# Kernel tuning notes

Measured on AMD Instinct MI355X. Metric: run time of the kernel, lower is better.

## Reference

```python
import jax, jax.numpy as jnp
import numpy as np

N, E, C1, E2, C2, B = 30000, 400000, 15000, 100000, 7500, 16
FV, FE, NC = 6, 3, 10


def _lin(k, i, o):
    kw, kb = jax.random.split(k)
    s = 1.0 / np.sqrt(i)
    w = jax.random.uniform(kw, (i, o), jnp.float32, -s, s)
    b = jax.random.uniform(kb, (o,), jnp.float32, -s, s)
    return w, b


def setup_inputs() -> dict:
    key = jax.random.key(0)
    ks = jax.random.split(key, 20)
    inp = {}
    inp["x"] = jax.random.normal(ks[0], (N, FV), jnp.float32)
    inp["edge_attr"] = jax.random.uniform(ks[1], (E, FE), jnp.float32)
    inp["pos"] = jax.random.uniform(ks[2], (N, 3), jnp.float32)
    inp["edge_index"] = jax.random.randint(ks[3], (2, E), 0, N)
    inp["batch"] = jnp.sort(jax.random.randint(ks[4], (N,), 0, B))
    inp["cluster1"] = jax.random.randint(ks[5], (N,), 0, C1)
    inp["edge_index2"] = jax.random.randint(ks[6], (2, E2), 0, C1)
    inp["cluster2"] = jax.random.randint(ks[7], (C1,), 0, C2)
    inp["w1a"], inp["b1a"] = _lin(ks[8], FE, 25)
    inp["w1b"], inp["b1b"] = _lin(ks[9], 25, 32 * FV)
    inp["root1"] = jax.random.normal(ks[10], (FV, 32), jnp.float32) / np.sqrt(FV)
    inp["bias1"] = jnp.zeros((32,), jnp.float32)
    inp["w2a"], inp["b2a"] = _lin(ks[11], 3, 25)
    inp["w2b"], inp["b2b"] = _lin(ks[12], 25, 32 * 64)
    inp["root2"] = jax.random.normal(ks[13], (32, 64), jnp.float32) / np.sqrt(32)
    inp["bias2"] = jnp.zeros((64,), jnp.float32)
    inp["fc1_w"], inp["fc1_b"] = _lin(ks[14], 64, 128)
    inp["fc2_w"], inp["fc2_b"] = _lin(ks[15], 128, NC)
    return inp


def _seg_mean(v, idx, n):
    s = jax.ops.segment_sum(v, idx, num_segments=n)
    c = jax.ops.segment_sum(jnp.ones(idx.shape, v.dtype), idx, num_segments=n)
    return s / jnp.maximum(c, 1.0)[:, None]


def _seg_max(v, idx, n):
    m = jax.ops.segment_max(v, idx, num_segments=n)
    return jnp.where(jnp.isfinite(m), m, 0.0)  # empty clusters -> 0


def _nnconv(x, src, dst, ea, wa, ba, wb, bb, root, bias, n, ci, co):
    # per-edge weight matrix from edge MLP: [E, ci, co]
    W = (jax.nn.relu(ea @ wa + ba) @ wb + bb).reshape(-1, ci, co)
    msg = jnp.einsum('ei,eio->eo', x[src], W)  # gather + per-edge matmul
    return _seg_mean(msg, dst, n) + x @ root + bias  # scatter-mean + root


def _cartesian(pos, src, dst):
    cart = pos[src] - pos[dst]
    return cart / (2.0 * jnp.max(jnp.abs(cart))) + 0.5  # T.Cartesian(norm=True)


def reference(x, edge_attr, pos, w1a, b1a, w1b, b1b, root1, bias1,
              w2a, b2a, w2b, b2b, root2, bias2, fc1_w, fc1_b, fc2_w, fc2_b,
              edge_index, batch, cluster1, edge_index2, cluster2):
    src1, dst1 = edge_index[0], edge_index[1]
    x1 = jax.nn.elu(_nnconv(x, src1, dst1, edge_attr, w1a, b1a, w1b, b1b,
                            root1, bias1, N, FV, 32))
    # max_pool with precomputed graclus cluster assignment
    xp = _seg_max(x1, cluster1, C1)
    posp = _seg_mean(pos, cluster1, C1)
    batchp = jnp.maximum(jax.ops.segment_max(batch, cluster1, num_segments=C1), 0)
    src2, dst2 = edge_index2[0], edge_index2[1]
    ea2 = _cartesian(posp, src2, dst2)
    x2 = jax.nn.elu(_nnconv(xp, src2, dst2, ea2, w2a, b2a, w2b, b2b,
                            root2, bias2, C1, 32, 64))
    # max_pool_x with second cluster assignment
    x3 = _seg_max(x2, cluster2, C2)
    batch2 = jnp.maximum(jax.ops.segment_max(batchp, cluster2, num_segments=C2), 0)
    g = _seg_mean(x3, batch2, B)  # global mean pool -> [B, 64]
    h = jax.nn.elu(g @ fc1_w + fc1_b)
    # dropout is identity in eval mode
    return jax.nn.log_softmax(h @ fc2_w + fc2_b, axis=1)
```

## Files before the change

kernel.cpp:

```cpp
#include <hip/hip_runtime.h>
#include <hip/hip_bf16.h>

#define Nn 30000
#define Ee 400000
#define C1n 15000
#define E2n 100000
#define C2n 7500
#define Bb 16

#define OFF_XPKEY   0
#define OFF_POSSUM  480000
#define OFF_CNTC1   525000
#define OFF_BPMAX   540000
#define OFF_X3KEY   555000
#define OFF_B2MAX   1035000
#define OFF_GSUM    1042500
#define OFF_GCNT    1043524
#define OFF_MAXABS  1043540
#define OFF_DEG1    1043544
#define OFF_FILL1   1073544
#define OFF_DEG2    1103544
#define OFF_FILL2   1118544
#define ZERO_ELEMS  1133544
#define OFF_RP1     1133544
#define OFF_RP2     1163548
#define OFF_POSP    1178552
#define OFF_XP      1223552
#define OFF_W1T     1703552
#define OFF_W2T     1707136
#define OFF_EA1R    1735808
#define OFF_C2R     3335808

typedef __attribute__((ext_vector_type(8))) short short8;
typedef __attribute__((ext_vector_type(4))) float f32x4;

__device__ __forceinline__ unsigned fkey(float f) {
    unsigned u = __float_as_uint(f);
    return (u >> 31) ? ~u : (u | 0x80000000u);
}
__device__ __forceinline__ float funkey(unsigned k) {
    unsigned u = (k >> 31) ? (k ^ 0x80000000u) : ~k;
    return __uint_as_float(u);
}
__device__ __forceinline__ float elu(float a) { return a > 0.f ? a : expm1f(a); }

__device__ __forceinline__ unsigned short f2bf(float f) {
    unsigned u = __float_as_uint(f);
    unsigned lsb = (u >> 16) & 1u;
    u += 0x7fffu + lsb;
    return (unsigned short)(u >> 16);
}

__global__ void hist_kernel(const int* __restrict__ ei, const int* __restrict__ ei2,
                            unsigned* __restrict__ deg1, unsigned* __restrict__ deg2) {
    int t = blockIdx.x * 256 + threadIdx.x;
    if (t < Ee) {
        atomicAdd(&deg1[ei[Ee + t]], 1u);
    } else if (t < Ee + E2n) {
        int e = t - Ee;
        atomicAdd(&deg2[ei2[E2n + e]], 1u);
    }
}

__global__ __launch_bounds__(1024) void scan_both(
    const unsigned* __restrict__ deg1, unsigned* __restrict__ rp1,
    const unsigned* __restrict__ deg2, unsigned* __restrict__ rp2) {
    const unsigned* deg; unsigned* rp; int n;
    if (blockIdx.x == 0) { deg = deg1; rp = rp1; n = Nn; }
    else                 { deg = deg2; rp = rp2; n = C1n; }
    __shared__ unsigned ps[1024];
    const int t = threadIdx.x;
    const int chunk = (n + 1023) / 1024;
    const int lo = t * chunk;
    const int hi = (lo + chunk < n) ? lo + chunk : n;
    unsigned s = 0;
    for (int i = lo; i < hi; ++i) s += deg[i];
    ps[t] = s;
    __syncthreads();
    for (int off = 1; off < 1024; off <<= 1) {
        unsigned v = (t >= off) ? ps[t - off] : 0u;
        __syncthreads();
        ps[t] += v;
        __syncthreads();
    }
    unsigned run = (t > 0) ? ps[t - 1] : 0u;
    if (t == 0) rp[0] = 0u;
    for (int i = lo; i < hi; ++i) { run += deg[i]; rp[i + 1] = run; }
}

__global__ void scatter1(const float* __restrict__ ea, const int* __restrict__ ei,
                         const unsigned* __restrict__ rp1, unsigned* __restrict__ fill1,
                         float4* __restrict__ EA1R) {
    int e = blockIdx.x * 256 + threadIdx.x;
    if (e >= Ee) return;
    int d = ei[Ee + e];
    unsigned p = rp1[d] + atomicAdd(&fill1[d], 1u);
    int src = ei[e];
    EA1R[p] = make_float4(ea[e * 3], ea[e * 3 + 1], ea[e * 3 + 2], __int_as_float(src));
}

__global__ void wt_kernel(const float* __restrict__ w1b, const float* __restrict__ b1b,
                          const float* __restrict__ root1, const float* __restrict__ bias1,
                          const float* __restrict__ w2b, const float* __restrict__ b2b,
                          const float* __restrict__ root2, const float* __restrict__ bias2,
                          unsigned short* __restrict__ W1T, unsigned short* __restrict__ W2T) {
    int t = blockIdx.x * 256 + threadIdx.x;
    if (t < 32 * 224) {
        int col = t / 224, p = t % 224;
        float v = 0.f;
        if (p < 208) {
            int k = p >> 3, i = p & 7;
            if (i < 6) v = (k < 25) ? w1b[k * 192 + i * 32 + col] : b1b[i * 32 + col];
        }
        else if (p < 214)  { v = root1[(p - 208) * 32 + col]; }
        else if (p == 214) { v = bias1[col]; }
        W1T[t] = f2bf(v);
    } else {
        int u = t - 32 * 224;
        if (u < 64 * 896) {
            int col = u / 896, p = u % 896;
            float v;
            if (p < 800)       { int k = p / 32, i = p % 32; v = w2b[k * 2048 + i * 64 + col]; }
            else if (p < 832)  { int i = p - 800; v = b2b[i * 64 + col]; }
            else if (p < 864)  { v = root2[(p - 832) * 64 + col]; }
            else if (p == 864) { v = bias2[col]; }
            else v = 0.f;
            W2T[u] = f2bf(v);
        }
    }
}

__global__ __launch_bounds__(256, 8) void g1conv1(
    const float* __restrict__ x, const float4* __restrict__ EA1R,
    const unsigned* __restrict__ rp1,
    const float* __restrict__ w1a, const float* __restrict__ b1a,
    const unsigned short* __restrict__ W1T,
    const float* __restrict__ pos, const int* __restrict__ batch, const int* __restrict__ cl1,
    unsigned* __restrict__ xpkey, float* __restrict__ possum,
    float* __restrict__ cntc1, int* __restrict__ bpmax) {
    __shared__ unsigned short As[16][232];
    const int tid = threadIdx.x;
    const int w = tid >> 6;
    const int l = tid & 63;
    const int m = l & 15, q = l >> 4;
    const int i8 = l & 7;
    const int kq = l >> 3;
    float wa0 = 0.f, wa1 = 0.f, wa2 = 0.f, ba0 = 0.f;
    if (l < 25) { wa0 = w1a[l]; wa1 = w1a[25 + l]; wa2 = w1a[50 + l]; ba0 = b1a[l]; }
    const int ntiles = Nn / 16;
    for (int tile = blockIdx.x; tile < ntiles; tile += gridDim.x) {
        const int base = tile * 16;
#pragma unroll
        for (int s4 = 0; s4 < 4; ++s4) {
            const int row = w * 4 + s4;
            const int d = base + row;
            const unsigned e0 = rp1[d], e1 = rp1[d + 1];
            float acc0 = 0.f, acc1 = 0.f, acc2 = 0.f, acc3 = 0.f;
            for (unsigned p = e0; p < e1; p += 4) {
                float4 ev[4];
                float xm[4];
#pragma unroll
                for (int b = 0; b < 4; ++b) {
                    const unsigned pp = (p + b < e1) ? p + b : e1 - 1;
                    ev[b] = EA1R[pp];
                }
#pragma unroll
                for (int b = 0; b < 4; ++b) {
                    const int sb = __float_as_int(ev[b].w) * 6;
                    xm[b] = (i8 < 6 && p + b < e1) ? x[sb + i8] : 0.f;
                }
#pragma unroll
                for (int b = 0; b < 4; ++b) {
                    float a = ba0 + ev[b].x * wa0 + ev[b].y * wa1 + ev[b].z * wa2;
                    float hown = (l == 25) ? 1.f : fmaxf(a, 0.f);
                    acc0 += __shfl(hown, kq, 64) * xm[b];
                    acc1 += __shfl(hown, 8 + kq, 64) * xm[b];
                    acc2 += __shfl(hown, 16 + kq, 64) * xm[b];
                    acc3 += __shfl(hown, 24 + kq, 64) * xm[b];
                }
            }
            const float dinv = 1.f / fmaxf((float)(e1 - e0), 1.f);
            As[row][l] = f2bf(acc0 * dinv);
            As[row][64 + l] = f2bf(acc1 * dinv);
            As[row][128 + l] = f2bf(acc2 * dinv);
            if (l < 16) {
                As[row][192 + l] = f2bf(acc3 * dinv);
                float tail;
                if (l < 6)       tail = x[d * 6 + l];
                else if (l == 6) tail = 1.f;
                else             tail = 0.f;
                As[row][208 + l] = f2bf(tail);
            }
        }
        __syncthreads();
        if (w < 2) {
            f32x4 acc = {0.f, 0.f, 0.f, 0.f};
#pragma unroll
            for (int s = 0; s < 7; ++s) {
                short8 av = *reinterpret_cast<const short8*>(&As[m][s * 32 + q * 8]);
                short8 bv = *reinterpret_cast<const short8*>(&W1T[(w * 16 + m) * 224 + s * 32 + q * 8]);
                acc = __builtin_amdgcn_mfma_f32_16x16x32_bf16(av, bv, acc, 0, 0, 0);
            }
#pragma unroll
            for (int r = 0; r < 4; ++r) {
                const int row = base + q * 4 + r;
                const int c = cl1[row];
                float v = elu(acc[r]);
                atomicMax(&xpkey[c * 32 + w * 16 + m], fkey(v));
            }
        } else if (w == 2) {
            if (l < 16) {
                const int row = base + l;
                const int c = cl1[row];
#pragma unroll
                for (int j = 0; j < 3; ++j) atomicAdd(&possum[c * 3 + j], pos[row * 3 + j]);
                atomicAdd(&cntc1[c], 1.f);
                atomicMax(&bpmax[c], batch[row]);
            }
        }
        __syncthreads();
    }
}

__global__ void pool1_final(const unsigned* __restrict__ xpkey, const float* __restrict__ possum,
                            const float* __restrict__ cntc1, float* __restrict__ xp,
                            float* __restrict__ posp) {
    int t = blockIdx.x * 256 + threadIdx.x;
    if (t >= C1n * 32) return;
    int c = t >> 5, o = t & 31;
    unsigned k = xpkey[t];
    xp[t] = k ? funkey(k) : 0.f;
    if (o < 3) posp[c * 3 + o] = possum[c * 3 + o] / fmaxf(cntc1[c], 1.f);
}

__global__ void scatter2(const float* __restrict__ posp, const int* __restrict__ ei2,
                         const unsigned* __restrict__ rp2, unsigned* __restrict__ fill2,
                         float4* __restrict__ C2R, unsigned* __restrict__ maxabs) {
    int e = blockIdx.x * 256 + threadIdx.x;
    float mx = 0.f;
    if (e < E2n) {
        int s = ei2[e], d = ei2[E2n + e];
        float c0 = posp[s * 3]     - posp[d * 3];
        float c1 = posp[s * 3 + 1] - posp[d * 3 + 1];
        float c2 = posp[s * 3 + 2] - posp[d * 3 + 2];
        mx = fmaxf(fmaxf(fabsf(c0), fabsf(c1)), fabsf(c2));
        unsigned p = rp2[d] + atomicAdd(&fill2[d], 1u);
        C2R[p] = make_float4(c0, c1, c2, __int_as_float(s));
    }
#pragma unroll
    for (int off = 32; off > 0; off >>= 1) mx = fmaxf(mx, __shfl_xor(mx, off));
    if ((threadIdx.x & 63) == 0) atomicMax(maxabs, __float_as_uint(mx));
}

__global__ __launch_bounds__(256, 5) void g2conv2(
    const float* __restrict__ xp, const float4* __restrict__ C2R,
    const unsigned* __restrict__ maxabs, const unsigned* __restrict__ rp2,
    const float* __restrict__ w2a, const float* __restrict__ b2a,
    const unsigned short* __restrict__ W2T,
    const int* __restrict__ cl2, const int* __restrict__ bpmax,
    unsigned* __restrict__ x3key, int* __restrict__ b2max) {
    __shared__ unsigned short As[16][904];
    const int tid = threadIdx.x;
    const int w = tid >> 6;
    const int l = tid & 63;
    const int m = l & 15, q = l >> 4;
    const int i = l & 31, hp = l >> 5;
    float wa0 = 0.f, wa1 = 0.f, wa2 = 0.f, ba0 = 0.f;
    if (l < 25) { wa0 = w2a[l]; wa1 = w2a[25 + l]; wa2 = w2a[50 + l]; ba0 = b2a[l]; }
    const float inv = 0.5f / __uint_as_float(maxabs[0]);
    const int ntiles = (C1n + 15) / 16;
    for (int tile = blockIdx.x; tile < ntiles; tile += gridDim.x) {
        const int base = tile * 16;
#pragma unroll
        for (int s4 = 0; s4 < 4; ++s4) {
            const int row = w * 4 + s4;
            const int d = base + row;
            if (d < C1n) {
                const unsigned e0 = rp2[d], e1 = rp2[d + 1];
                float acc[13];
#pragma unroll
                for (int r = 0; r < 13; ++r) acc[r] = 0.f;
                for (unsigned p = e0; p < e1; p += 4) {
                    float4 cv[4];
                    float xv[4];
#pragma unroll
                    for (int b = 0; b < 4; ++b) {
                        const unsigned pp = (p + b < e1) ? p + b : e1 - 1;
                        cv[b] = C2R[pp];
                    }
#pragma unroll
                    for (int b = 0; b < 4; ++b)
                        xv[b] = (p + b < e1) ? xp[__float_as_int(cv[b].w) * 32 + i] : 0.f;
#pragma unroll
                    for (int b = 0; b < 4; ++b) {
                        float a = ba0 + (cv[b].x * inv + 0.5f) * wa0 + (cv[b].y * inv + 0.5f) * wa1
                                      + (cv[b].z * inv + 0.5f) * wa2;
                        float hown = (l == 25) ? 1.f : fmaxf(a, 0.f);
#pragma unroll
                        for (int r = 0; r < 13; ++r)
                            acc[r] += __shfl(hown, 2 * r + hp, 64) * xv[b];
                    }
                }
                const float dinv = 1.f / fmaxf((float)(e1 - e0), 1.f);
#pragma unroll
                for (int r = 0; r < 13; ++r) As[row][r * 64 + l] = f2bf(acc[r] * dinv);
                As[row][832 + l] = f2bf((l < 32) ? xp[d * 32 + l] : (l == 32 ? 1.f : 0.f));
                if (l == 0) atomicMax(&b2max[cl2[d]], bpmax[d]);
            } else {
#pragma unroll
                for (int r = 0; r < 13; ++r) As[row][r * 64 + l] = 0;
                As[row][832 + l] = 0;
            }
        }
        __syncthreads();
        {
            f32x4 a4 = {0.f, 0.f, 0.f, 0.f};
#pragma unroll 4
            for (int s = 0; s < 28; ++s) {
                short8 av = *reinterpret_cast<const short8*>(&As[m][s * 32 + q * 8]);
                short8 bv = *reinterpret_cast<const short8*>(&W2T[(w * 16 + m) * 896 + s * 32 + q * 8]);
                a4 = __builtin_amdgcn_mfma_f32_16x16x32_bf16(av, bv, a4, 0, 0, 0);
            }
#pragma unroll
            for (int r = 0; r < 4; ++r) {
                const int row = base + q * 4 + r;
                if (row < C1n) {
                    const int c2 = cl2[row];
                    float v = elu(a4[r]);
                    atomicMax(&x3key[c2 * 64 + w * 16 + m], fkey(v));
                }
            }
        }
        __syncthreads();
    }
}

__global__ __launch_bounds__(256) void gacc_kernel(
    const unsigned* __restrict__ x3key, const int* __restrict__ b2max,
    float* __restrict__ gsum, float* __restrict__ gcnt) {
    __shared__ float ls[Bb * 64];
    __shared__ float lc[Bb];
    const int t = threadIdx.x;
    for (int i = t; i < Bb * 64; i += 256) ls[i] = 0.f;
    if (t < Bb) lc[t] = 0.f;
    __syncthreads();
    const int o = t & 63;
    const int cs = t >> 6;
    for (int c = blockIdx.x * 4 + cs; c < C2n; c += gridDim.x * 4) {
        int b = b2max[c];
        unsigned k = x3key[c * 64 + o];
        float v = k ? funkey(k) : 0.f;
        atomicAdd(&ls[b * 64 + o], v);
        if (o == 0) atomicAdd(&lc[b], 1.f);
    }
    __syncthreads();
    for (int i = t; i < Bb * 64; i += 256) {
        float v = ls[i];
        if (v != 0.f) atomicAdd(&gsum[i], v);
    }
    if (t < Bb) {
        float v = lc[t];
        if (v != 0.f) atomicAdd(&gcnt[t], v);
    }
}

__global__ void head_kernel(const float* __restrict__ gsum, const float* __restrict__ gcnt,
                            const float* __restrict__ fc1w, const float* __restrict__ fc1b,
                            const float* __restrict__ fc2w, const float* __restrict__ fc2b,
                            float* __restrict__ out) {
    __shared__ float g[16 * 64];
    __shared__ float hb[16 * 128];
    __shared__ float lg[16 * 10];
    __shared__ float rowm[16];
    int t = threadIdx.x;
    for (int idx = t; idx < 16 * 64; idx += 256) {
        int b = idx >> 6;
        g[idx] = gsum[idx] / fmaxf(gcnt[b], 1.f);
    }
    __syncthreads();
    for (int idx = t; idx < 16 * 128; idx += 256) {
        int b = idx >> 7, j = idx & 127;
        float a = fc1b[j];
        for (int i = 0; i < 64; ++i) a += g[b * 64 + i] * fc1w[i * 128 + j];
        hb[idx] = elu(a);
    }
    __syncthreads();
    for (int idx = t; idx < 160; idx += 256) {
        int b = idx / 10, c = idx % 10;
        float a = fc2b[c];
        for (int i = 0; i < 128; ++i) a += hb[b * 128 + i] * fc2w[i * 10 + c];
        lg[idx] = a;
    }
    __syncthreads();
    if (t < 16) {
        float m = -1e30f;
        for (int c = 0; c < 10; ++c) m = fmaxf(m, lg[t * 10 + c]);
        float s = 0.f;
        for (int c = 0; c < 10; ++c) s += expf(lg[t * 10 + c] - m);
        rowm[t] = m + logf(s);
    }
    __syncthreads();
    for (int idx = t; idx < 160; idx += 256) out[idx] = lg[idx] - rowm[idx / 10];
}

extern "C" void kernel_launch(void* const* d_in, const int* in_sizes, int n_in,
                              void* d_out, int out_size, void* d_ws, size_t ws_size,
                              hipStream_t stream) {
    const float* x     = (const float*)d_in[0];
    const float* ea    = (const float*)d_in[1];
    const float* pos   = (const float*)d_in[2];
    const int*   ei    = (const int*)d_in[3];
    const int*   batch = (const int*)d_in[4];
    const int*   cl1   = (const int*)d_in[5];
    const int*   ei2   = (const int*)d_in[6];
    const int*   cl2   = (const int*)d_in[7];
    const float* w1a   = (const float*)d_in[8];
    const float* b1a   = (const float*)d_in[9];
    const float* w1b   = (const float*)d_in[10];
    const float* b1b   = (const float*)d_in[11];
    const float* root1 = (const float*)d_in[12];
    const float* bias1 = (const float*)d_in[13];
    const float* w2a   = (const float*)d_in[14];
    const float* b2a   = (const float*)d_in[15];
    const float* w2b   = (const float*)d_in[16];
    const float* b2b   = (const float*)d_in[17];
    const float* root2 = (const float*)d_in[18];
    const float* bias2 = (const float*)d_in[19];
    const float* fc1w  = (const float*)d_in[20];
    const float* fc1b  = (const float*)d_in[21];
    const float* fc2w  = (const float*)d_in[22];
    const float* fc2b  = (const float*)d_in[23];
    float* out = (float*)d_out;

    float* ws = (float*)d_ws;
    unsigned* xpkey  = (unsigned*)(ws + OFF_XPKEY);
    float*    possum = ws + OFF_POSSUM;
    float*    cntc1  = ws + OFF_CNTC1;
    int*      bpmax  = (int*)(ws + OFF_BPMAX);
    unsigned* x3key  = (unsigned*)(ws + OFF_X3KEY);
    int*      b2max  = (int*)(ws + OFF_B2MAX);
    float*    gsum   = ws + OFF_GSUM;
    float*    gcnt   = ws + OFF_GCNT;
    unsigned* maxabs = (unsigned*)(ws + OFF_MAXABS);
    unsigned* deg1   = (unsigned*)(ws + OFF_DEG1);
    unsigned* fill1  = (unsigned*)(ws + OFF_FILL1);
    unsigned* deg2   = (unsigned*)(ws + OFF_DEG2);
    unsigned* fill2  = (unsigned*)(ws + OFF_FILL2);
    unsigned* rp1    = (unsigned*)(ws + OFF_RP1);
    unsigned* rp2    = (unsigned*)(ws + OFF_RP2);
    float*    posp   = ws + OFF_POSP;
    float*    xp     = ws + OFF_XP;
    unsigned short* W1T = (unsigned short*)(ws + OFF_W1T);
    unsigned short* W2T = (unsigned short*)(ws + OFF_W2T);
    float4*   EA1R  = (float4*)(ws + OFF_EA1R);
    float4*   C2R   = (float4*)(ws + OFF_C2R);

    hipMemsetAsync(ws, 0, (size_t)ZERO_ELEMS * 4, stream);

    wt_kernel<<<252, 256, 0, stream>>>(w1b, b1b, root1, bias1, w2b, b2b, root2, bias2, W1T, W2T);
    hist_kernel<<<(Ee + E2n + 255) / 256, 256, 0, stream>>>(ei, ei2, deg1, deg2);
    scan_both<<<2, 1024, 0, stream>>>(deg1, rp1, deg2, rp2);
    scatter1<<<(Ee + 255) / 256, 256, 0, stream>>>(ea, ei, rp1, fill1, EA1R);
    g1conv1<<<1875, 256, 0, stream>>>(x, EA1R, rp1, w1a, b1a, W1T, pos, batch, cl1,
                                      xpkey, possum, cntc1, bpmax);
    pool1_final<<<(C1n * 32 + 255) / 256, 256, 0, stream>>>(xpkey, possum, cntc1, xp, posp);
    scatter2<<<(E2n + 255) / 256, 256, 0, stream>>>(posp, ei2, rp2, fill2, C2R, maxabs);
    g2conv2<<<938, 256, 0, stream>>>(xp, C2R, maxabs, rp2, w2a, b2a, W2T, cl2, bpmax,
                                     x3key, b2max);
    gacc_kernel<<<32, 256, 0, stream>>>(x3key, b2max, gsum, gcnt);
    head_kernel<<<1, 256, 0, stream>>>(gsum, gcnt, fc1w, fc1b, fc2w, fc2b, out);
}
```

Baseline: 340.3 us.

## Pre-gather source node features into CSR-ordered edge buffers during scatter

The scatter kernels now copy each edge's source-node features (x for conv1, pooled xp for conv2) into edge-sorted buffers laid out in CSR order. The conv kernels then read these features contiguously instead of doing a dependent random gather through the source index stored in the edge record. This takes the dependent load latency out of the conv inner loops. In exchange it adds large extra writes (8 floats per edge for conv1, 32 floats per edge for conv2), and the random gathers still happen, only moved into the scatter kernels.

```diff
diff --git a/kernel.cpp b/kernel.cpp
--- a/kernel.cpp
+++ b/kernel.cpp
@@ -30,6 +30,8 @@
 #define OFF_W2T     1707136
 #define OFF_EA1R    1735808
 #define OFF_C2R     3335808
+#define OFF_X1R     3735808
+#define OFF_XP2R    6935808
 
 typedef __attribute__((ext_vector_type(8))) short short8;
 typedef __attribute__((ext_vector_type(4))) float f32x4;
@@ -88,15 +90,19 @@
     for (int i = lo; i < hi; ++i) { run += deg[i]; rp[i + 1] = run; }
 }
 
-__global__ void scatter1(const float* __restrict__ ea, const int* __restrict__ ei,
+__global__ void scatter1(const float* __restrict__ x, const float* __restrict__ ea,
+                         const int* __restrict__ ei,
                          const unsigned* __restrict__ rp1, unsigned* __restrict__ fill1,
-                         float4* __restrict__ EA1R) {
+                         float4* __restrict__ EA1R, float4* __restrict__ X1R) {
     int e = blockIdx.x * 256 + threadIdx.x;
     if (e >= Ee) return;
     int d = ei[Ee + e];
     unsigned p = rp1[d] + atomicAdd(&fill1[d], 1u);
     int src = ei[e];
-    EA1R[p] = make_float4(ea[e * 3], ea[e * 3 + 1], ea[e * 3 + 2], __int_as_float(src));
+    EA1R[p] = make_float4(ea[e * 3], ea[e * 3 + 1], ea[e * 3 + 2], 0.f);
+    const float* xs = x + (size_t)src * 6;
+    X1R[p * 2]     = make_float4(xs[0], xs[1], xs[2], xs[3]);
+    X1R[p * 2 + 1] = make_float4(xs[4], xs[5], 0.f, 0.f);
 }
 
 __global__ void wt_kernel(const float* __restrict__ w1b, const float* __restrict__ b1b,
@@ -131,8 +137,8 @@
 }
 
 __global__ __launch_bounds__(256, 8) void g1conv1(
-    const float* __restrict__ x, const float4* __restrict__ EA1R,
-    const unsigned* __restrict__ rp1,
+    const float4* __restrict__ EA1R, const float* __restrict__ X1Rf,
+    const float* __restrict__ x, const unsigned* __restrict__ rp1,
     const float* __restrict__ w1a, const float* __restrict__ b1a,
     const unsigned short* __restrict__ W1T,
     const float* __restrict__ pos, const int* __restrict__ batch, const int* __restrict__ cl1,
@@ -163,11 +169,8 @@
                 for (int b = 0; b < 4; ++b) {
                     const unsigned pp = (p + b < e1) ? p + b : e1 - 1;
                     ev[b] = EA1R[pp];
-                }
-#pragma unroll
-                for (int b = 0; b < 4; ++b) {
-                    const int sb = __float_as_int(ev[b].w) * 6;
-                    xm[b] = (i8 < 6 && p + b < e1) ? x[sb + i8] : 0.f;
+                    float xv = X1Rf[(size_t)pp * 8 + i8];
+                    xm[b] = (p + b < e1) ? xv : 0.f;
                 }
 #pragma unroll
                 for (int b = 0; b < 4; ++b) {
@@ -233,9 +236,11 @@
     if (o < 3) posp[c * 3 + o] = possum[c * 3 + o] / fmaxf(cntc1[c], 1.f);
 }
 
-__global__ void scatter2(const float* __restrict__ posp, const int* __restrict__ ei2,
+__global__ void scatter2(const float* __restrict__ posp, const float* __restrict__ xp,
+                         const int* __restrict__ ei2,
                          const unsigned* __restrict__ rp2, unsigned* __restrict__ fill2,
-                         float4* __restrict__ C2R, unsigned* __restrict__ maxabs) {
+                         float4* __restrict__ C2R, float4* __restrict__ XP2R,
+                         unsigned* __restrict__ maxabs) {
     int e = blockIdx.x * 256 + threadIdx.x;
     float mx = 0.f;
     if (e < E2n) {
@@ -245,7 +250,11 @@
         float c2 = posp[s * 3 + 2] - posp[d * 3 + 2];
         mx = fmaxf(fmaxf(fabsf(c0), fabsf(c1)), fabsf(c2));
         unsigned p = rp2[d] + atomicAdd(&fill2[d], 1u);
-        C2R[p] = make_float4(c0, c1, c2, __int_as_float(s));
+        C2R[p] = make_float4(c0, c1, c2, 0.f);
+        const float4* xs = reinterpret_cast<const float4*>(xp + (size_t)s * 32);
+        float4* xd = XP2R + (size_t)p * 8;
+#pragma unroll
+        for (int j = 0; j < 8; ++j) xd[j] = xs[j];
     }
 #pragma unroll
     for (int off = 32; off > 0; off >>= 1) mx = fmaxf(mx, __shfl_xor(mx, off));
@@ -253,7 +262,8 @@
 }
 
 __global__ __launch_bounds__(256, 5) void g2conv2(
-    const float* __restrict__ xp, const float4* __restrict__ C2R,
+    const float4* __restrict__ C2R, const float* __restrict__ XP2Rf,
+    const float* __restrict__ xp,
     const unsigned* __restrict__ maxabs, const unsigned* __restrict__ rp2,
     const float* __restrict__ w2a, const float* __restrict__ b2a,
     const unsigned short* __restrict__ W2T,
@@ -287,10 +297,9 @@
                     for (int b = 0; b < 4; ++b) {
                         const unsigned pp = (p + b < e1) ? p + b : e1 - 1;
                         cv[b] = C2R[pp];
+                        float xl = XP2Rf[(size_t)pp * 32 + i];
+                        xv[b] = (p + b < e1) ? xl : 0.f;
                     }
-#pragma unroll
-                    for (int b = 0; b < 4; ++b)
-                        xv[b] = (p + b < e1) ? xp[__float_as_int(cv[b].w) * 32 + i] : 0.f;
 #pragma unroll
                     for (int b = 0; b < 4; ++b) {
                         float a = ba0 + (cv[b].x * inv + 0.5f) * wa0 + (cv[b].y * inv + 0.5f) * wa1
@@ -454,18 +463,21 @@
     unsigned short* W2T = (unsigned short*)(ws + OFF_W2T);
     float4*   EA1R  = (float4*)(ws + OFF_EA1R);
     float4*   C2R   = (float4*)(ws + OFF_C2R);
+    float*    X1R   = ws + OFF_X1R;
+    float*    XP2R  = ws + OFF_XP2R;
 
     hipMemsetAsync(ws, 0, (size_t)ZERO_ELEMS * 4, stream);
 
     wt_kernel<<<252, 256, 0, stream>>>(w1b, b1b, root1, bias1, w2b, b2b, root2, bias2, W1T, W2T);
     hist_kernel<<<(Ee + E2n + 255) / 256, 256, 0, stream>>>(ei, ei2, deg1, deg2);
     scan_both<<<2, 1024, 0, stream>>>(deg1, rp1, deg2, rp2);
-    scatter1<<<(Ee + 255) / 256, 256, 0, stream>>>(ea, ei, rp1, fill1, EA1R);
-    g1conv1<<<1875, 256, 0, stream>>>(x, EA1R, rp1, w1a, b1a, W1T, pos, batch, cl1,
+    scatter1<<<(Ee + 255) / 256, 256, 0, stream>>>(x, ea, ei, rp1, fill1, EA1R, (float4*)X1R);
+    g1conv1<<<1875, 256, 0, stream>>>(EA1R, X1R, x, rp1, w1a, b1a, W1T, pos, batch, cl1,
                                       xpkey, possum, cntc1, bpmax);
     pool1_final<<<(C1n * 32 + 255) / 256, 256, 0, stream>>>(xpkey, possum, cntc1, xp, posp);
-    scatter2<<<(E2n + 255) / 256, 256, 0, stream>>>(posp, ei2, rp2, fill2, C2R, maxabs);
-    g2conv2<<<938, 256, 0, stream>>>(xp, C2R, maxabs, rp2, w2a, b2a, W2T, cl2, bpmax,
+    scatter2<<<(E2n + 255) / 256, 256, 0, stream>>>(posp, xp, ei2, rp2, fill2, C2R,
+                                                    (float4*)XP2R, maxabs);
+    g2conv2<<<938, 256, 0, stream>>>(C2R, XP2R, xp, maxabs, rp2, w2a, b2a, W2T, cl2, bpmax,
                                      x3key, b2max);
     gacc_kernel<<<32, 256, 0, stream>>>(x3key, b2max, gsum, gcnt);
     head_kernel<<<1, 256, 0, stream>>>(gsum, gcnt, fc1w, fc1b, fc2w, fc2b, out);
```

After: 334.7 us. No clear change (-1.7%).
